# Kernel tuning notes

Hardware: AMD Instinct MI355X
Metric: run time of the kernel (lower is better)

## Reference

```python
import jax, jax.numpy as jnp
import numpy as np

NUM_HEADS = 8
WINDOW = 8


def setup_inputs() -> dict:
    key = jax.random.key(0)
    k1, k2, k3, k4 = jax.random.split(key, 4)
    B, H, W, C = 8, 192, 192, 192
    x = jax.random.normal(k1, (B, H * W, C), dtype=jnp.float32)
    w_qkv = jax.random.normal(k2, (C, 3 * C), dtype=jnp.float32) * 0.02
    w_proj = jax.random.normal(k3, (C, C), dtype=jnp.float32) * 0.02
    b_proj = jax.random.normal(k4, (C,), dtype=jnp.float32) * 0.02
    return {"x": x, "w_qkv": w_qkv, "w_proj": w_proj, "b_proj": b_proj, "H": H, "W": W}


def reference(x, w_qkv, w_proj, b_proj, H, W):
    B, L, C = x.shape
    N = WINDOW * WINDOW  # 64 tokens per window
    Nw = L // N          # number of windows (torch view chain == flat reshape, no permute)
    scale = (C // NUM_HEADS) ** -0.5
    # qkv projection on flat tokens, then window reshape
    qkv = (x @ w_qkv).reshape(B, Nw, N, 3, C)
    q = qkv[..., 0, :]
    k = qkv[..., 1, :] * scale
    v = qkv[..., 2, :]
    # channel attention: [B,Nw,C,C]
    attn = jnp.einsum('bwnc,bwnd->bwcd', k, v)
    attn = jax.nn.softmax(attn, axis=-1)
    # out[b,w,n,c] = sum_d attn[b,w,c,d] * q[b,w,n,d]
    out = jnp.einsum('bwcd,bwnd->bwnc', attn, q)
    out = out.reshape(B, L, C)
    return out @ w_proj + b_proj
```

## Files before the change

kernel.cpp:

```cpp
#include <hip/hip_runtime.h>
#include <hip/hip_bf16.h>

typedef short bf16x8 __attribute__((ext_vector_type(8)));
typedef float f32x4  __attribute__((ext_vector_type(4)));

__device__ __forceinline__ unsigned short f2bf(float f) {
  unsigned int u = __float_as_uint(f);
  u += 0x7fffu + ((u >> 16) & 1u);
  return (unsigned short)(u >> 16);
}

__device__ __forceinline__ f32x4 fzero() { f32x4 z = {0.f, 0.f, 0.f, 0.f}; return z; }

#define WQKV_FRAGS (6*36*64)
#define WP_FRAGS   (6*12*64)
#define WQKV_ELEMS (WQKV_FRAGS*8)

__global__ void prepack_weights(const float* __restrict__ wqkv,
                                const float* __restrict__ wproj,
                                unsigned short* __restrict__ ws) {
  int t = blockIdx.x * 256 + threadIdx.x;
  const float scale = 0.20412414523193154f;
  if (t < WQKV_FRAGS) {
    int kt  = t / (36*64);
    int rem = t - kt*(36*64);
    int nt  = rem >> 6;
    int l   = rem & 63;
    int n   = nt*16 + (l & 15);
    int k0  = kt*32 + (l >> 4)*8;
    float s = (n >= 192 && n < 384) ? scale : 1.0f;
    union { unsigned short us[8]; uint4 v; } u;
#pragma unroll
    for (int j = 0; j < 8; ++j) u.us[j] = f2bf(wqkv[(k0 + j)*576 + n] * s);
    *(uint4*)(ws + (size_t)t * 8) = u.v;
  } else if (t < WQKV_FRAGS + WP_FRAGS) {
    int t2  = t - WQKV_FRAGS;
    int kt  = t2 / (12*64);
    int rem = t2 - kt*(12*64);
    int nt  = rem >> 6;
    int l   = rem & 63;
    int n   = nt*16 + (l & 15);
    int k0  = kt*32 + (l >> 4)*8;
    union { unsigned short us[8]; uint4 v; } u;
#pragma unroll
    for (int j = 0; j < 8; ++j) u.us[j] = f2bf(wproj[(k0 + j)*192 + n]);
    *(uint4*)(ws + (size_t)WQKV_ELEMS + (size_t)t2 * 8) = u.v;
  }
}

__launch_bounds__(768, 3)
__global__ void win_attn_fused(const float* __restrict__ x,
                               const unsigned short* __restrict__ wqkv_sw,
                               const unsigned short* __restrict__ wp_sw,
                               const float* __restrict__ bias,
                               float* __restrict__ out) {
  __shared__ __align__(16) unsigned char smem[156672];
  unsigned short* sX    = (unsigned short*)(smem);
  unsigned short* sQ    = (unsigned short*)(smem + 25600);
  unsigned short* sKt   = (unsigned short*)(smem + 51200);
  unsigned short* sVt   = (unsigned short*)(smem + 78848);
  float*          sAttn = (float*)(smem + 106496);
  unsigned short* sOut  = (unsigned short*)(smem);

  const int tid  = threadIdx.x;
  const int lane = tid & 63;
  const int wv   = tid >> 6;
  const int l16  = lane & 15;
  const int lq   = lane >> 4;

  {
    const float4* xg = (const float4*)(x + (size_t)blockIdx.x * 12288);
#pragma unroll
    for (int i = 0; i < 4; ++i) {
      int idx = tid + i * 768;
      float4 v = xg[idx];
      int e = idx << 2;
      unsigned short* p = sX + (e / 192) * 200 + (e % 192);
      p[0] = f2bf(v.x); p[1] = f2bf(v.y); p[2] = f2bf(v.z); p[3] = f2bf(v.w);
    }
  }
  __syncthreads();

  {
    bf16x8 af[4][6];
#pragma unroll
    for (int ms = 0; ms < 4; ++ms)
#pragma unroll
      for (int kt = 0; kt < 6; ++kt)
        af[ms][kt] = *(const bf16x8*)(sX + (ms*16 + l16)*200 + kt*32 + lq*8);

    for (int nt = wv; nt < 36; nt += 12) {
      f32x4 acc[4] = {fzero(), fzero(), fzero(), fzero()};
      const bf16x8* bp = (const bf16x8*)wqkv_sw + nt*64 + lane;
#pragma unroll
      for (int kt = 0; kt < 6; ++kt) {
        bf16x8 b = bp[kt * (36*64)];
#pragma unroll
        for (int ms = 0; ms < 4; ++ms)
          acc[ms] = __builtin_amdgcn_mfma_f32_16x16x32_bf16(af[ms][kt], b, acc[ms], 0, 0, 0);
      }
      int c = nt*16 + l16;
#pragma unroll
      for (int ms = 0; ms < 4; ++ms) {
        int rb = ms*16 + lq*4;
        if (c < 192) {
#pragma unroll
          for (int r = 0; r < 4; ++r) sQ[(rb + r)*200 + c] = f2bf(acc[ms][r]);
        } else if (c < 384) {
#pragma unroll
          for (int r = 0; r < 4; ++r) sKt[(c - 192)*72 + rb + r] = f2bf(acc[ms][r]);
        } else {
#pragma unroll
          for (int r = 0; r < 4; ++r) sVt[(c - 384)*72 + rb + r] = f2bf(acc[ms][r]);
        }
      }
    }
  }
  __syncthreads();

  f32x4 accF[4];
#pragma unroll
  for (int m = 0; m < 4; ++m) accF[m] = fzero();

  for (int cb = 0; cb < 3; ++cb) {
    {
      bf16x8 ak[4][2];
#pragma unroll
      for (int ms = 0; ms < 4; ++ms)
#pragma unroll
        for (int kt = 0; kt < 2; ++kt)
          ak[ms][kt] = *(const bf16x8*)(sKt + (cb*64 + ms*16 + l16)*72 + kt*32 + lq*8);
      int dt = wv;
      f32x4 acc[4] = {fzero(), fzero(), fzero(), fzero()};
#pragma unroll
      for (int kt = 0; kt < 2; ++kt) {
        bf16x8 b = *(const bf16x8*)(sVt + (dt*16 + l16)*72 + kt*32 + lq*8);
#pragma unroll
        for (int ms = 0; ms < 4; ++ms)
          acc[ms] = __builtin_amdgcn_mfma_f32_16x16x32_bf16(ak[ms][kt], b, acc[ms], 0, 0, 0);
      }
      int d = dt*16 + l16;
#pragma unroll
      for (int ms = 0; ms < 4; ++ms)
#pragma unroll
        for (int r = 0; r < 4; ++r)
          sAttn[(ms*16 + lq*4 + r)*196 + d] = acc[ms][r];
    }
    __syncthreads();

    if (tid < 512) {
      int row = tid >> 3, seg = tid & 7;
      float* rp = sAttn + row*196 + seg;
      float v0[24];
      float mx = -3.0e38f;
#pragma unroll
      for (int i = 0; i < 24; ++i) { v0[i] = rp[i*8]; mx = fmaxf(mx, v0[i]); }
      mx = fmaxf(mx, __shfl_xor(mx, 1));
      mx = fmaxf(mx, __shfl_xor(mx, 2));
      mx = fmaxf(mx, __shfl_xor(mx, 4));
      float s = 0.f;
#pragma unroll
      for (int i = 0; i < 24; ++i) { float e = __expf(v0[i] - mx); v0[i] = e; s += e; }
      s += __shfl_xor(s, 1);
      s += __shfl_xor(s, 2);
      s += __shfl_xor(s, 4);
      float inv = 1.0f / s;
#pragma unroll
      for (int i = 0; i < 24; ++i) rp[i*8] = v0[i] * inv;
    }
    __syncthreads();

    if (wv < 8) {
      int ct = wv & 3, mh = wv >> 2;
      bf16x8 aq[2][6];
#pragma unroll
      for (int mi = 0; mi < 2; ++mi)
#pragma unroll
        for (int kt = 0; kt < 6; ++kt)
          aq[mi][kt] = *(const bf16x8*)(sQ + ((mh*2 + mi)*16 + l16)*200 + kt*32 + lq*8);
      f32x4 acc[2] = {fzero(), fzero()};
#pragma unroll
      for (int kt = 0; kt < 6; ++kt) {
        const float* ap = sAttn + (ct*16 + l16)*196 + kt*32 + lq*8;
        float4 f0 = *(const float4*)ap;
        float4 f1 = *(const float4*)(ap + 4);
        bf16x8 b;
        b[0] = (short)f2bf(f0.x); b[1] = (short)f2bf(f0.y);
        b[2] = (short)f2bf(f0.z); b[3] = (short)f2bf(f0.w);
        b[4] = (short)f2bf(f1.x); b[5] = (short)f2bf(f1.y);
        b[6] = (short)f2bf(f1.z); b[7] = (short)f2bf(f1.w);
#pragma unroll
        for (int mi = 0; mi < 2; ++mi)
          acc[mi] = __builtin_amdgcn_mfma_f32_16x16x32_bf16(aq[mi][kt], b, acc[mi], 0, 0, 0);
      }
#pragma unroll
      for (int mi = 0; mi < 2; ++mi)
#pragma unroll
        for (int r = 0; r < 4; ++r)
          sOut[((mh*2 + mi)*16 + lq*4 + r)*72 + ct*16 + l16] = f2bf(acc[mi][r]);
    }
    __syncthreads();

    {
      bf16x8 ao[4][2];
#pragma unroll
      for (int ms = 0; ms < 4; ++ms)
#pragma unroll
        for (int kt = 0; kt < 2; ++kt)
          ao[ms][kt] = *(const bf16x8*)(sOut + (ms*16 + l16)*72 + kt*32 + lq*8);
      const bf16x8* bp = (const bf16x8*)wp_sw + ((cb*2)*12 + wv)*64 + lane;
#pragma unroll
      for (int kt = 0; kt < 2; ++kt) {
        bf16x8 b = bp[kt * (12*64)];
#pragma unroll
        for (int ms = 0; ms < 4; ++ms)
          accF[ms] = __builtin_amdgcn_mfma_f32_16x16x32_bf16(ao[ms][kt], b, accF[ms], 0, 0, 0);
      }
    }
  }

  {
    int e = wv*16 + l16;
    float bv = bias[e];
    float* op = out + (size_t)blockIdx.x * 12288;
#pragma unroll
    for (int ms = 0; ms < 4; ++ms)
#pragma unroll
      for (int r = 0; r < 4; ++r)
        op[(ms*16 + lq*4 + r)*192 + e] = accF[ms][r] + bv;
  }
}

extern "C" void kernel_launch(void* const* d_in, const int* in_sizes, int n_in,
                              void* d_out, int out_size, void* d_ws, size_t ws_size,
                              hipStream_t stream) {
  const float* x     = (const float*)d_in[0];
  const float* wqkv  = (const float*)d_in[1];
  const float* wproj = (const float*)d_in[2];
  const float* bproj = (const float*)d_in[3];
  unsigned short* ws = (unsigned short*)d_ws;

  int nwin = in_sizes[0] / 12288;

  prepack_weights<<<72, 256, 0, stream>>>(wqkv, wproj, ws);
  win_attn_fused<<<nwin, 768, 0, stream>>>(x, ws, ws + WQKV_ELEMS, bproj, (float*)d_out);
}
```

Measured before the change: 581.2 us.

## Fuse softmax into attention-logit MFMA registers and store bf16 probabilities

Logits are now computed transposed (V as the A operand, K columns as B), so each wave holds a full column slice of one channel row. Softmax max and sum are reduced in registers with shuffles and a small cross-wave float2 exchange, and the result is written once as bf16. This removes the fp32 sAttn buffer, the separate softmax pass with its extra barrier, and the fp32-to-bf16 conversion in the next GEMM. It also cuts LDS from about 153KB to 115KB, and hoists the V and Q fragment loads out of the cb loop. The trade-off is higher register pressure from the hoisted fragments.

```diff
diff --git a/kernel.cpp b/kernel.cpp
--- a/kernel.cpp
+++ b/kernel.cpp
@@ -54,13 +54,14 @@
                                const unsigned short* __restrict__ wp_sw,
                                const float* __restrict__ bias,
                                float* __restrict__ out) {
-  __shared__ __align__(16) unsigned char smem[156672];
-  unsigned short* sX    = (unsigned short*)(smem);
-  unsigned short* sQ    = (unsigned short*)(smem + 25600);
-  unsigned short* sKt   = (unsigned short*)(smem + 51200);
-  unsigned short* sVt   = (unsigned short*)(smem + 78848);
-  float*          sAttn = (float*)(smem + 106496);
-  unsigned short* sOut  = (unsigned short*)(smem);
+  __shared__ __align__(16) unsigned char smem[117248];
+  unsigned short* sX   = (unsigned short*)(smem);
+  unsigned short* sP   = (unsigned short*)(smem);
+  unsigned short* sQ   = (unsigned short*)(smem + 25600);
+  unsigned short* sKt  = (unsigned short*)(smem + 51200);
+  unsigned short* sVt  = (unsigned short*)(smem + 78848);
+  unsigned short* sOut = (unsigned short*)(smem + 106496);
+  float2*         sRed = (float2*)(smem + 115712);
 
   const int tid  = threadIdx.x;
   const int lane = tid & 63;
@@ -122,73 +123,80 @@
 #pragma unroll
   for (int m = 0; m < 4; ++m) accF[m] = fzero();
 
+  const int ccs = wv & 3;
+  const int thr = wv >> 2;
+
+  bf16x8 av[4][2];
+#pragma unroll
+  for (int mi = 0; mi < 4; ++mi)
+#pragma unroll
+    for (int kt = 0; kt < 2; ++kt) {
+      int rd = thr*64 + mi*16 + l16;
+      av[mi][kt] = *(const bf16x8*)(sVt + rd*72 + kt*32 + lq*8);
+    }
+
+  const int ct = wv & 3, mh = wv >> 2;
+  bf16x8 aq[2][6];
+  if (wv < 8) {
+#pragma unroll
+    for (int mi = 0; mi < 2; ++mi)
+#pragma unroll
+      for (int kt = 0; kt < 6; ++kt)
+        aq[mi][kt] = *(const bf16x8*)(sQ + ((mh*2 + mi)*16 + l16)*200 + kt*32 + lq*8);
+  }
+
   for (int cb = 0; cb < 3; ++cb) {
+    f32x4 lac[4] = {fzero(), fzero(), fzero(), fzero()};
     {
-      bf16x8 ak[4][2];
-#pragma unroll
-      for (int ms = 0; ms < 4; ++ms)
-#pragma unroll
-        for (int kt = 0; kt < 2; ++kt)
-          ak[ms][kt] = *(const bf16x8*)(sKt + (cb*64 + ms*16 + l16)*72 + kt*32 + lq*8);
-      int dt = wv;
-      f32x4 acc[4] = {fzero(), fzero(), fzero(), fzero()};
+      int rc = cb*64 + ccs*16 + l16;
 #pragma unroll
       for (int kt = 0; kt < 2; ++kt) {
-        bf16x8 b = *(const bf16x8*)(sVt + (dt*16 + l16)*72 + kt*32 + lq*8);
-#pragma unroll
-        for (int ms = 0; ms < 4; ++ms)
-          acc[ms] = __builtin_amdgcn_mfma_f32_16x16x32_bf16(ak[ms][kt], b, acc[ms], 0, 0, 0);
-      }
-      int d = dt*16 + l16;
-#pragma unroll
-      for (int ms = 0; ms < 4; ++ms)
-#pragma unroll
-        for (int r = 0; r < 4; ++r)
-          sAttn[(ms*16 + lq*4 + r)*196 + d] = acc[ms][r];
+        bf16x8 b = *(const bf16x8*)(sKt + rc*72 + kt*32 + lq*8);
+#pragma unroll
+        for (int mi = 0; mi < 4; ++mi)
+          lac[mi] = __builtin_amdgcn_mfma_f32_16x16x32_bf16(av[mi][kt], b, lac[mi], 0, 0, 0);
+      }
+    }
+
+    int ccl = ccs*16 + l16;
+    {
+      float l[16];
+#pragma unroll
+      for (int mi = 0; mi < 4; ++mi)
+#pragma unroll
+        for (int r = 0; r < 4; ++r) l[mi*4+r] = lac[mi][r];
+      float mx = l[0];
+#pragma unroll
+      for (int i = 1; i < 16; ++i) mx = fmaxf(mx, l[i]);
+      mx = fmaxf(mx, __shfl_xor(mx, 16));
+      mx = fmaxf(mx, __shfl_xor(mx, 32));
+      float s = 0.f;
+#pragma unroll
+      for (int i = 0; i < 16; ++i) { float e = __expf(l[i] - mx); l[i] = e; s += e; }
+      s += __shfl_xor(s, 16);
+      s += __shfl_xor(s, 32);
+      if (lane < 16) sRed[thr*64 + ccl] = make_float2(mx, s);
+      __syncthreads();
+      float2 r0 = sRed[ccl], r1 = sRed[64 + ccl], r2 = sRed[128 + ccl];
+      float M = fmaxf(fmaxf(r0.x, r1.x), r2.x);
+      float S = r0.y*__expf(r0.x - M) + r1.y*__expf(r1.x - M) + r2.y*__expf(r2.x - M);
+      float sc = __expf(mx - M) / S;
+#pragma unroll
+      for (int mi = 0; mi < 4; ++mi) {
+        int d0 = thr*64 + mi*16 + lq*4;
+        union { unsigned short us[4]; uint2 v; } u;
+        u.us[0] = f2bf(l[mi*4+0]*sc); u.us[1] = f2bf(l[mi*4+1]*sc);
+        u.us[2] = f2bf(l[mi*4+2]*sc); u.us[3] = f2bf(l[mi*4+3]*sc);
+        *(uint2*)(sP + ccl*200 + d0) = u.v;
+      }
     }
     __syncthreads();
 
-    if (tid < 512) {
-      int row = tid >> 3, seg = tid & 7;
-      float* rp = sAttn + row*196 + seg;
-      float v0[24];
-      float mx = -3.0e38f;
-#pragma unroll
-      for (int i = 0; i < 24; ++i) { v0[i] = rp[i*8]; mx = fmaxf(mx, v0[i]); }
-      mx = fmaxf(mx, __shfl_xor(mx, 1));
-      mx = fmaxf(mx, __shfl_xor(mx, 2));
-      mx = fmaxf(mx, __shfl_xor(mx, 4));
-      float s = 0.f;
-#pragma unroll
-      for (int i = 0; i < 24; ++i) { float e = __expf(v0[i] - mx); v0[i] = e; s += e; }
-      s += __shfl_xor(s, 1);
-      s += __shfl_xor(s, 2);
-      s += __shfl_xor(s, 4);
-      float inv = 1.0f / s;
-#pragma unroll
-      for (int i = 0; i < 24; ++i) rp[i*8] = v0[i] * inv;
-    }
-    __syncthreads();
-
     if (wv < 8) {
-      int ct = wv & 3, mh = wv >> 2;
-      bf16x8 aq[2][6];
-#pragma unroll
-      for (int mi = 0; mi < 2; ++mi)
-#pragma unroll
-        for (int kt = 0; kt < 6; ++kt)
-          aq[mi][kt] = *(const bf16x8*)(sQ + ((mh*2 + mi)*16 + l16)*200 + kt*32 + lq*8);
       f32x4 acc[2] = {fzero(), fzero()};
 #pragma unroll
       for (int kt = 0; kt < 6; ++kt) {
-        const float* ap = sAttn + (ct*16 + l16)*196 + kt*32 + lq*8;
-        float4 f0 = *(const float4*)ap;
-        float4 f1 = *(const float4*)(ap + 4);
-        bf16x8 b;
-        b[0] = (short)f2bf(f0.x); b[1] = (short)f2bf(f0.y);
-        b[2] = (short)f2bf(f0.z); b[3] = (short)f2bf(f0.w);
-        b[4] = (short)f2bf(f1.x); b[5] = (short)f2bf(f1.y);
-        b[6] = (short)f2bf(f1.z); b[7] = (short)f2bf(f1.w);
+        bf16x8 b = *(const bf16x8*)(sP + (ct*16 + l16)*200 + kt*32 + lq*8);
 #pragma unroll
         for (int mi = 0; mi < 2; ++mi)
           acc[mi] = __builtin_amdgcn_mfma_f32_16x16x32_bf16(aq[mi][kt], b, acc[mi], 0, 0, 0);
```

Result: faster. 518.4 us (-10.8%).
